# Performance work log

Hardware: AMD Instinct MI355X
Metric: run time of the kernel (lower is better)

Reference implementation:

```python
import jax, jax.numpy as jnp
from jax import lax
import numpy as np

LRELU_SLOPE = 0.01  # PyTorch LeakyReLU default
BETA = 0.25


def lrelu(x):
    return jnp.where(x >= 0, x, LRELU_SLOPE * x)


def conv2d(x, w, b, stride, pad):
    # x: [B,C,H,W], w: [Cout,Cin,k,k] (torch OIHW)
    y = lax.conv_general_dilated(x, w, (stride, stride), ((pad, pad), (pad, pad)),
                                 dimension_numbers=('NCHW', 'OIHW', 'NCHW'))
    return y + b[None, :, None, None]


def conv_transpose2d(x, w, b, stride, out_pad):
    # w: torch ConvTranspose2d weight [Cin,Cout,k,k]; implement as dilated conv
    # with spatially flipped kernel. out = (i-1)*stride + k + out_pad.
    wf = jnp.flip(w, (2, 3)).transpose(1, 0, 2, 3)  # -> [Cout,Cin,k,k]
    k = w.shape[2]
    pad = ((k - 1, k - 1 + out_pad), (k - 1, k - 1 + out_pad))
    y = lax.conv_general_dilated(x, wf, (1, 1), pad, lhs_dilation=(stride, stride),
                                 dimension_numbers=('NCHW', 'OIHW', 'NCHW'))
    return y + b[None, :, None, None]


def setup_inputs() -> dict:
    key = jax.random.key(0)
    ks = jax.random.split(key, 16)
    s = 0.05
    inp = {
        'x':   jax.random.normal(ks[0], (64, 1, 256, 256), jnp.float32),
        'ew1': jax.random.normal(ks[1], (8, 1, 4, 4), jnp.float32) * s,
        'eb1': jnp.zeros((8,), jnp.float32),
        'ew2': jax.random.normal(ks[2], (16, 8, 4, 4), jnp.float32) * s,
        'eb2': jnp.zeros((16,), jnp.float32),
        'ew3': jax.random.normal(ks[3], (32, 16, 4, 4), jnp.float32) * s,
        'eb3': jnp.zeros((32,), jnp.float32),
        'ew4': jax.random.normal(ks[4], (32, 32, 3, 3), jnp.float32) * s,
        'eb4': jnp.zeros((32,), jnp.float32),
        'ew5': jax.random.normal(ks[5], (64, 32, 1, 1), jnp.float32) * s,
        'eb5': jnp.zeros((64,), jnp.float32),
        'dw1': jax.random.normal(ks[6], (32, 64, 3, 3), jnp.float32) * s,
        'db1': jnp.zeros((32,), jnp.float32),
        'dw2': jax.random.normal(ks[7], (32, 16, 4, 4), jnp.float32) * s,
        'db2': jnp.zeros((16,), jnp.float32),
        'dw3': jax.random.normal(ks[8], (16, 8, 4, 4), jnp.float32) * s,
        'db3': jnp.zeros((8,), jnp.float32),
        'dw4': jax.random.normal(ks[9], (8, 1, 4, 4), jnp.float32) * s,
        'db4': jnp.zeros((1,), jnp.float32),
        # nn.init.uniform_(-1/K, 1/K) with K=512
        'codebook': jax.random.uniform(ks[10], (512, 64), jnp.float32,
                                       minval=-1.0 / 512, maxval=1.0 / 512),
    }
    return inp


def vqvae_forward(x, ew1, eb1, ew2, eb2, ew3, eb3, ew4, eb4, ew5, eb5,
                  dw1, db1, dw2, db2, dw3, db3, dw4, db4, codebook):
    # ---- encoder ----
    h = lrelu(conv2d(x, ew1, eb1, 2, 0))   # [B,8,127,127]
    h = lrelu(conv2d(h, ew2, eb2, 2, 0))   # [B,16,62,62]
    h = lrelu(conv2d(h, ew3, eb3, 2, 0))   # [B,32,30,30]
    h = lrelu(conv2d(h, ew4, eb4, 1, 1))   # [B,32,30,30]
    h = lrelu(conv2d(h, ew5, eb5, 1, 0))   # [B,64,30,30]
    # ---- vector quantizer ----
    lat = h.transpose(0, 2, 3, 1)                      # [B,h,w,D]
    D = lat.shape[-1]
    flat = lat.reshape(-1, D)                          # [N,D]
    # squared euclidean distances via expansion (same argmin as torch.norm)
    d2 = (jnp.sum(flat * flat, axis=1, keepdims=True)
          - 2.0 * flat @ codebook.T
          + jnp.sum(codebook * codebook, axis=1))      # [N,K]
    idx = jnp.argmin(d2, axis=1)                       # [N]
    q = codebook[idx].reshape(lat.shape)               # [B,h,w,D]
    commitment = jnp.mean((lax.stop_gradient(q) - lat) ** 2)
    embedding = jnp.mean((q - lax.stop_gradient(lat)) ** 2)
    vq_loss = commitment * BETA + embedding
    q_st = lat + lax.stop_gradient(q - lat)            # straight-through
    z = q_st.transpose(0, 3, 1, 2)                     # [B,D,h,w]
    # ---- decoder ----
    h = lrelu(conv2d(z, dw1, db1, 1, 1))               # [B,32,30,30]
    h = lrelu(conv_transpose2d(h, dw2, db2, 2, 1))     # [B,16,63,63]
    h = lrelu(conv_transpose2d(h, dw3, db3, 2, 1))     # [B,8,131,131]
    recons = jnp.tanh(conv_transpose2d(h, dw4, db4, 2, 0))  # [B,1,264,264]
    return recons, vq_loss


def reference(x, ew1, eb1, ew2, eb2, ew3, eb3, ew4, eb4, ew5, eb5,
              dw1, db1, dw2, db2, dw3, db3, dw4, db4, codebook):
    return vqvae_forward(x, ew1, eb1, ew2, eb2, ew3, eb3, ew4, eb4, ew5, eb5,
                         dw1, db1, dw2, db2, dw3, db3, dw4, db4, codebook)
```

## Files before the change

### kernel.cpp

```cpp
#include <hip/hip_runtime.h>
#include <hip/hip_bf16.h>
#include <math.h>

#define LRELU 0.01f

template<int NW>
__device__ __forceinline__ void ldw(const float* p, float* w) {
    if constexpr (NW % 4 == 0) {
#pragma unroll
        for (int u = 0; u < NW / 4; u++) {
            float4 v = *(const float4*)(p + 4 * u);
            w[4*u] = v.x; w[4*u+1] = v.y; w[4*u+2] = v.z; w[4*u+3] = v.w;
        }
    } else {
#pragma unroll
        for (int c = 0; c < NW; c++) w[c] = p[c];
    }
}

__device__ __forceinline__ void wfwd(const float* s, float* d, int CIN, int COUT,
                                     int KK, int i) {
    int co = i / (CIN * KK); int r = i - co * CIN * KK;
    int ci = r / KK; int t = r - ci * KK;
    d[(ci * KK + t) * COUT + co] = s[i];
}
__device__ __forceinline__ void wtr(const float* s, float* d, int CIN, int COUT,
                                    int KK, int i) {
    int ci = i / (COUT * KK); int r = i - ci * COUT * KK;
    int co = r / KK; int t = r - co * KK;
    d[(t * CIN + ci) * COUT + co] = s[i];
}
__global__ __launch_bounds__(256)
void prep_k(const float* e1, const float* e2, const float* e3, const float* e4,
            const float* e5, const float* d1, const float* d2, const float* d3,
            const float* d4, float* w, const float* cbp, float* hcbn,
            unsigned long long* keys, float* loss, int* idxm, int N) {
    int i = blockIdx.x * 256 + threadIdx.x;
    if      (i < 128)   wfwd(e1, w + 0,     1,  8, 16, i);
    else if (i < 2176)  wfwd(e2, w + 128,   8, 16, 16, i - 128);
    else if (i < 10368) wfwd(e3, w + 2176, 16, 32, 16, i - 2176);
    else if (i < 19584) wfwd(e4, w + 10368, 32, 32, 9, i - 10368);
    else if (i < 21632) wfwd(e5, w + 19584, 32, 64, 1, i - 19584);
    else if (i < 40064) wfwd(d1, w + 21632, 64, 32, 9, i - 21632);
    else if (i < 48256) wtr (d2, w + 40064, 32, 16, 16, i - 40064);
    else if (i < 50304) wtr (d3, w + 48256, 16,  8, 16, i - 48256);
    else if (i < 50432) wtr (d4, w + 50304,  8,  1, 16, i - 50304);
    else if (i < 50944) {
        int k = i - 50432;
        const float* c = cbp + k * 64;
        float s = 0.f;
#pragma unroll
        for (int d = 0; d < 64; d++) s = fmaf(c[d], c[d], s);
        hcbn[k] = 0.5f * s;
    } else if (i < 50944 + N) {
        keys[i - 50944] = 0xFFFFFFFFFFFFFFFFull;
    } else if (i == 50944 + N) {
        loss[0] = 0.f;
    } else if (i < 50945 + N + 64 * 124) {
        int j = i - (50945 + N);
        int b2 = j / 124, s = j - b2 * 124;
        int r, c;
        if (s < 32)      { r = 0;  c = s; }
        else if (s < 64) { r = 31; c = s - 32; }
        else { int u = s - 64; r = 1 + (u >> 1); c = (u & 1) * 31; }
        idxm[b2 * 1024 + r * 32 + c] = 512;
    }
}

__global__ __launch_bounds__(256)
void ubuild_k(const float* __restrict__ w, const float* __restrict__ cb,
              float* __restrict__ U) {
    int g = blockIdx.x * 256 + threadIdx.x;
    if (g >= 513 * 288) return;
    if (g >= 512 * 288) { U[g] = 0.f; return; }
    int k = g / 288, rem = g - k * 288;
    const float* cr = cb + k * 64;
    float s = 0.f;
#pragma unroll 4
    for (int ci = 0; ci < 64; ci++)
        s = fmaf(w[ci * 288 + rem], cr[ci], s);
    U[g] = s;
}

template<int CIN, int COUT, int CO_BLK, int HIN, int ISTR, int HOUT, int WOUT,
         int OPLANE, int OSTR, int OPAD, int CB, int RB, int ZCONV, int ZF_CH>
__global__ __launch_bounds__(256)
void convs2_k(const float* __restrict__ in, const float* __restrict__ wt,
              const float* __restrict__ bias, float* __restrict__ out) {
    const int b = blockIdx.x, cog = blockIdx.y, tid = threadIdx.x;
    if (ZF_CH > 0 && (int)blockIdx.z >= ZCONV) {
        if (cog != 0) return;
        int i = ((int)blockIdx.z - ZCONV) * 256 + tid;
        if (i >= ZF_CH * 124) return;
        int ch = i / 124, s = i - ch * 124;
        int r, c;
        if (s < 32)      { r = 0;  c = s; }
        else if (s < 64) { r = 31; c = s - 32; }
        else { int u = s - 64; r = 1 + (u >> 1); c = (u & 1) * 31; }
        out[(size_t)(b * ZF_CH + ch) * 1024 + r * 32 + c] = 0.f;
        return;
    }
    __shared__ __align__(16) float lw[CIN * 16 * CO_BLK];
    for (int i = tid; i < CIN * 16 * CO_BLK; i += 256) {
        int row = i / CO_BLK, c = i - row * CO_BLK;
        lw[i] = wt[row * COUT + cog * CO_BLK + c];
    }
    __syncthreads();

    const int tz = blockIdx.z;
    const int cbi = tz / RB, rb = tz - cbi * RB;
    const int tx = tid & 15, ty = tid >> 4;
    const int ow0 = (cbi * 16 + tx) * 2;
    const int oh  = rb * 16 + ty;
    if (oh >= HOUT || ow0 >= WOUT) return;
    const bool p1v = (ow0 + 1) < WOUT;

    float acc[CO_BLK][2];
#pragma unroll
    for (int c = 0; c < CO_BLK; c++) {
        float bv = bias[cog * CO_BLK + c];
        acc[c][0] = bv; acc[c][1] = bv;
    }
    const float* inb = in + ((size_t)(b * CIN) * HIN + oh * 2) * ISTR + ow0 * 2;
#pragma unroll 2
    for (int ci = 0; ci < CIN; ci++) {
        const float* r = inb + (size_t)ci * HIN * ISTR;
        float4 a4[4]; float2 b2[4];
#pragma unroll
        for (int kh = 0; kh < 4; kh++) {
            a4[kh] = *(const float4*)(r + kh * ISTR);
            b2[kh] = p1v ? *(const float2*)(r + kh * ISTR + 4) : make_float2(0.f, 0.f);
        }
        const float* wr = lw + ci * 16 * CO_BLK;
#pragma unroll
        for (int kh = 0; kh < 4; kh++) {
            float x0[4] = {a4[kh].x, a4[kh].y, a4[kh].z, a4[kh].w};
            float x1[4] = {a4[kh].z, a4[kh].w, b2[kh].x, b2[kh].y};
#pragma unroll
            for (int kw = 0; kw < 4; kw++) {
                float wv[CO_BLK];
                ldw<CO_BLK>(wr + (kh * 4 + kw) * CO_BLK, wv);
#pragma unroll
                for (int c = 0; c < CO_BLK; c++) {
                    acc[c][0] = fmaf(x0[kw], wv[c], acc[c][0]);
                    acc[c][1] = fmaf(x1[kw], wv[c], acc[c][1]);
                }
            }
        }
    }
    float* ob = out + (size_t)(b * COUT + cog * CO_BLK) * OPLANE
                    + (oh + OPAD) * OSTR + ow0 + OPAD;
#pragma unroll
    for (int c = 0; c < CO_BLK; c++) {
        float v0 = acc[c][0]; v0 = (v0 >= 0.f) ? v0 : LRELU * v0;
        ob[(size_t)c * OPLANE] = v0;
        if (p1v) {
            float v1 = acc[c][1]; v1 = (v1 >= 0.f) ? v1 : LRELU * v1;
            ob[(size_t)c * OPLANE + 1] = v1;
        }
    }
}

template<int CIN, int COUT, int CO_BLK, int OPLANE, int OSTR, int OPADH, int OPADV,
         bool ZSIDE>
__global__ __launch_bounds__(256)
void conv3_k(const float* __restrict__ in, const float* __restrict__ wt,
             const float* __restrict__ bias, float* __restrict__ out) {
    const int b = blockIdx.x, cog = blockIdx.y, tid = threadIdx.x;
    __shared__ __align__(16) float lw[CIN * 9 * CO_BLK];
    for (int i = tid; i < CIN * 9 * CO_BLK; i += 256) {
        int row = i / CO_BLK, c = i - row * CO_BLK;
        lw[i] = wt[row * COUT + cog * CO_BLK + c];
    }
    __syncthreads();

    const int rb = blockIdx.z;
    const int tx = tid & 15, ty = tid >> 4;
    const int r = rb * 16 + ty;
    if (r >= 30) return;
    const int ow0 = tx * 2;
    if (tx == 15) {
        if (ZSIDE) {
#pragma unroll
            for (int c = 0; c < CO_BLK; c++) {
                float* base = out + (size_t)(b * COUT + cog * CO_BLK + c) * OPLANE
                                  + (r + OPADV) * OSTR;
                base[0] = 0.f; base[31] = 0.f; base[32] = 0.f;
            }
        }
        return;
    }
    float acc[CO_BLK][2];
#pragma unroll
    for (int c = 0; c < CO_BLK; c++) {
        float bv = bias[cog * CO_BLK + c];
        acc[c][0] = bv; acc[c][1] = bv;
    }
    const float* inb = in + ((size_t)(b * CIN) * 32 + r) * 32 + ow0;
#pragma unroll 2
    for (int ci = 0; ci < CIN; ci++) {
        const float* rr = inb + (size_t)ci * 1024;
        float2 A[3], Bv[3];
#pragma unroll
        for (int kh = 0; kh < 3; kh++) {
            A[kh]  = *(const float2*)(rr + kh * 32);
            Bv[kh] = *(const float2*)(rr + kh * 32 + 2);
        }
        const float* wr = lw + ci * 9 * CO_BLK;
#pragma unroll
        for (int kh = 0; kh < 3; kh++) {
            float x0[3] = {A[kh].x, A[kh].y, Bv[kh].x};
            float x1[3] = {A[kh].y, Bv[kh].x, Bv[kh].y};
#pragma unroll
            for (int kw = 0; kw < 3; kw++) {
                float wv[CO_BLK];
                ldw<CO_BLK>(wr + (kh * 3 + kw) * CO_BLK, wv);
#pragma unroll
                for (int c = 0; c < CO_BLK; c++) {
                    acc[c][0] = fmaf(x0[kw], wv[c], acc[c][0]);
                    acc[c][1] = fmaf(x1[kw], wv[c], acc[c][1]);
                }
            }
        }
    }
    float* ob = out + (size_t)(b * COUT + cog * CO_BLK) * OPLANE
                    + (r + OPADV) * OSTR + ow0 + OPADH;
#pragma unroll
    for (int c = 0; c < CO_BLK; c++) {
        float v0 = acc[c][0]; v0 = (v0 >= 0.f) ? v0 : LRELU * v0;
        float v1 = acc[c][1]; v1 = (v1 >= 0.f) ? v1 : LRELU * v1;
        ob[(size_t)c * OPLANE] = v0;
        ob[(size_t)c * OPLANE + 1] = v1;
    }
}

template<int CIN, int COUT, int CO_BLK>
__global__ __launch_bounds__(256)
void conv1_k(const float* __restrict__ in, const float* __restrict__ wt,
             const float* __restrict__ bias, float* __restrict__ out) {
    __shared__ __align__(16) float lw[CIN * CO_BLK];
    const int b = blockIdx.x, cog = blockIdx.y;
    for (int i = threadIdx.x; i < CIN * CO_BLK; i += 256) {
        int row = i / CO_BLK, c = i - row * CO_BLK;
        lw[i] = wt[row * COUT + cog * CO_BLK + c];
    }
    __syncthreads();

    const int px4 = threadIdx.x * 4;
    float acc[CO_BLK][4];
#pragma unroll
    for (int c = 0; c < CO_BLK; c++) {
        float bv = bias[cog * CO_BLK + c];
        acc[c][0] = bv; acc[c][1] = bv; acc[c][2] = bv; acc[c][3] = bv;
    }
#pragma unroll 4
    for (int ci = 0; ci < CIN; ci++) {
        float4 x = *(const float4*)(in + (size_t)(b * CIN + ci) * 1024 + px4);
        float wv[CO_BLK];
        ldw<CO_BLK>(lw + ci * CO_BLK, wv);
#pragma unroll
        for (int c = 0; c < CO_BLK; c++) {
            acc[c][0] = fmaf(x.x, wv[c], acc[c][0]);
            acc[c][1] = fmaf(x.y, wv[c], acc[c][1]);
            acc[c][2] = fmaf(x.z, wv[c], acc[c][2]);
            acc[c][3] = fmaf(x.w, wv[c], acc[c][3]);
        }
    }
#pragma unroll
    for (int c = 0; c < CO_BLK; c++) {
        float4 v;
        v.x = (acc[c][0] >= 0.f) ? acc[c][0] : LRELU * acc[c][0];
        v.y = (acc[c][1] >= 0.f) ? acc[c][1] : LRELU * acc[c][1];
        v.z = (acc[c][2] >= 0.f) ? acc[c][2] : LRELU * acc[c][2];
        v.w = (acc[c][3] >= 0.f) ? acc[c][3] : LRELU * acc[c][3];
        *(float4*)(out + (size_t)(b * COUT + cog * CO_BLK + c) * 1024 + px4) = v;
    }
}

__global__ __launch_bounds__(256)
void d1tab_k(const int* __restrict__ idxm, const float* __restrict__ U,
             const float* __restrict__ bias, float* __restrict__ out) {
    const int b = blockIdx.x, cog = blockIdx.y, rt = blockIdx.z;
    const int tx = threadIdx.x & 31, ty = threadIdx.x >> 5;
    const int r = rt * 8 + ty;
    if (r >= 30) return;
    if (tx >= 30) {
        if (tx == 31) {
#pragma unroll
            for (int c = 0; c < 16; c++) {
                float* base = out + (size_t)(b * 32 + cog * 16 + c) * 1020 + r * 34;
                base[1] = 0.f; base[32] = 0.f; base[33] = 0.f;
            }
        }
        return;
    }
    const int* im = idxm + b * 1024 + r * 32 + tx;
    float acc[16];
#pragma unroll
    for (int c = 0; c < 16; c++) acc[c] = bias[cog * 16 + c];
#pragma unroll
    for (int kh = 0; kh < 3; kh++) {
        int i0 = im[kh * 32 + 0];
        int i1 = im[kh * 32 + 1];
        int i2 = im[kh * 32 + 2];
        const float4* u0 = (const float4*)(U + ((size_t)i0 * 9 + kh * 3 + 0) * 32 + cog * 16);
        const float4* u1 = (const float4*)(U + ((size_t)i1 * 9 + kh * 3 + 1) * 32 + cog * 16);
        const float4* u2 = (const float4*)(U + ((size_t)i2 * 9 + kh * 3 + 2) * 32 + cog * 16);
#pragma unroll
        for (int q = 0; q < 4; q++) {
            float4 a = u0[q], bb = u1[q], cc = u2[q];
            acc[4*q+0] += (a.x + bb.x) + cc.x;
            acc[4*q+1] += (a.y + bb.y) + cc.y;
            acc[4*q+2] += (a.z + bb.z) + cc.z;
            acc[4*q+3] += (a.w + bb.w) + cc.w;
        }
    }
    float* ob = out + (size_t)(b * 32 + cog * 16) * 1020 + r * 34 + tx + 2;
#pragma unroll
    for (int c = 0; c < 16; c++) {
        float v = acc[c]; v = (v >= 0.f) ? v : LRELU * v;
        ob[(size_t)c * 1020] = v;
    }
}

template<int CIN, int COUT, int CO_BLK, int HIN, int ISTR, int HOUT, int WOUT,
         int OPLANE, int OSTR, int OPADH, int NTX, int NT,
         int ZS_CH, int ZS_H, int ZS_STR, int ZC0, int ZC1, int ZC2,
         bool DO_TANH, bool DO_LOSS>
__global__ __launch_bounds__(256)
void convtf_k(const float* __restrict__ in, const float* __restrict__ wt,
              const float* __restrict__ bias, float* __restrict__ out,
              const float* __restrict__ loss, float* __restrict__ losstgt) {
    const int b = blockIdx.x, tid = threadIdx.x;
    const int NCOG = COUT / CO_BLK;
    int zz = blockIdx.z;
    if (zz >= NCOG * NT) {
        if (DO_LOSS) {
            if (b == 0 && tid == 0)
                losstgt[0] = 1.25f * loss[0] / (57600.f * 64.f);
            return;
        }
        int i = (zz - NCOG * NT) * 256 + tid;
        if (i >= ZS_CH * ZS_H * 3) return;
        int ch = i / (ZS_H * 3); int u = i - ch * ZS_H * 3;
        int r = u / 3, c3 = u - r * 3;
        int col = (c3 == 0) ? ZC0 : (c3 == 1) ? ZC1 : ZC2;
        out[((size_t)(b * ZS_CH + ch) * ZS_H + r) * ZS_STR + col] = 0.f;
        return;
    }
    const int cog = zz / NT, tile = zz - cog * NT;
    const int tlx = tile % NTX, tly = tile / NTX;

    __shared__ __align__(16) float lw[16 * CIN * CO_BLK];
    for (int i = tid; i < 16 * CIN * CO_BLK; i += 256) {
        int aq = i / (CIN * 4 * CO_BLK);
        int r1 = i - aq * (CIN * 4 * CO_BLK);
        int ci = r1 / (4 * CO_BLK);
        int u  = r1 - ci * (4 * CO_BLK);
        int pp = u / CO_BLK, c = u - pp * CO_BLK;
        int a = aq >> 1, q = aq & 1, py = pp >> 1, px = pp & 1;
        int tap = (py + 2 * a) * 4 + px + 2 * q;
        lw[i] = wt[((size_t)tap * CIN + ci) * COUT + cog * CO_BLK + c];
    }
    __syncthreads();

    const int SX = (WOUT + 1) >> 1, SY = (HOUT + 1) >> 1;
    const int sx0 = tlx * 32 + (tid & 15);
    const int sx1 = sx0 + 16;
    const int sy  = tly * 16 + (tid >> 4);
    const bool v0 = sx0 < SX, v1 = sx1 < SX;
    if (sy >= SY || !(v0 || v1)) return;

    const bool rvA = (sy < HIN);
    const bool rvB = (sy >= 1) && (sy <= HIN);

    float acc[2][4][CO_BLK];
#pragma unroll
    for (int s = 0; s < 2; s++)
#pragma unroll
        for (int o = 0; o < 4; o++)
#pragma unroll
            for (int c = 0; c < CO_BLK; c++)
                acc[s][o][c] = bias[cog * CO_BLK + c];

    const float* base = in + (size_t)(b * CIN) * HIN * ISTR;
#pragma unroll 2
    for (int ci = 0; ci < CIN; ci++) {
        const float* rowA = base + (size_t)ci * HIN * ISTR + (size_t)sy * ISTR;
        const float* rowB = rowA - ISTR;
        float rA0x = 0.f, rA0y = 0.f, rA1x = 0.f, rA1y = 0.f;
        float rB0x = 0.f, rB0y = 0.f, rB1x = 0.f, rB1y = 0.f;
        if (rvA) {
            if (v0) { rA0x = rowA[sx0]; rA0y = rowA[sx0 + 1]; }
            if (v1) { rA1x = rowA[sx1]; rA1y = rowA[sx1 + 1]; }
        }
        if (rvB) {
            if (v0) { rB0x = rowB[sx0]; rB0y = rowB[sx0 + 1]; }
            if (v1) { rB1x = rowB[sx1]; rB1y = rowB[sx1 + 1]; }
        }
#pragma unroll
        for (int a = 0; a < 2; a++) {
#pragma unroll
            for (int q = 0; q < 2; q++) {
                float iv0 = q ? (a ? rB0x : rA0x) : (a ? rB0y : rA0y);
                float iv1 = q ? (a ? rB1x : rA1x) : (a ? rB1y : rA1y);
                const float* wp = lw + (size_t)((a * 2 + q) * CIN + ci) * (4 * CO_BLK);
                float wv[4 * CO_BLK];
                ldw<4 * CO_BLK>(wp, wv);
#pragma unroll
                for (int o = 0; o < 4; o++)
#pragma unroll
                    for (int c = 0; c < CO_BLK; c++) {
                        acc[0][o][c] = fmaf(iv0, wv[o * CO_BLK + c], acc[0][o][c]);
                        acc[1][o][c] = fmaf(iv1, wv[o * CO_BLK + c], acc[1][o][c]);
                    }
            }
        }
    }
#pragma unroll
    for (int s = 0; s < 2; s++) {
        if (s ? !v1 : !v0) continue;
        const int sxx = s ? sx1 : sx0;
        const int ow = 2 * sxx;
        const bool full = (ow + 1) < WOUT;
#pragma unroll
        for (int py = 0; py < 2; py++) {
            int oh = 2 * sy + py;
            if (oh >= HOUT) continue;
            float* ob = out + (size_t)(b * COUT + cog * CO_BLK) * OPLANE
                            + (size_t)oh * OSTR + ow + OPADH;
#pragma unroll
            for (int c = 0; c < CO_BLK; c++) {
                float va = acc[s][py * 2 + 0][c];
                float vb = acc[s][py * 2 + 1][c];
                if (DO_TANH) { va = tanhf(va); vb = tanhf(vb); }
                else {
                    va = (va >= 0.f) ? va : LRELU * va;
                    vb = (vb >= 0.f) ? vb : LRELU * vb;
                }
                if ((OPADH & 1) == 0 && full) {
                    *(float2*)(ob + (size_t)c * OPLANE) = make_float2(va, vb);
                } else {
                    ob[(size_t)c * OPLANE] = va;
                    if (full) ob[(size_t)c * OPLANE + 1] = vb;
                }
            }
        }
    }
}

__global__ __launch_bounds__(256)
void vq_argmin_k(const float* __restrict__ lat, const float* __restrict__ cb,
                 const float* __restrict__ hcbn,
                 unsigned long long* __restrict__ keys) {
    const int pb = blockIdx.x;
    if (pb >= 225) return;
    __shared__ float4 scb4[1024];
    __shared__ float  shn[64];
    const int tid = threadIdx.x;
    const int dq  = tid & 3;
    const int pg  = tid >> 2;
    const int kbase = blockIdx.y * 64;
    const int posbase = pb * 256;

    const float4* src = (const float4*)(cb + (size_t)kbase * 64);
#pragma unroll
    for (int i = 0; i < 4; i++) scb4[tid + 256 * i] = src[tid + 256 * i];
    if (tid < 64) shn[tid] = hcbn[kbase + tid];

    float l[4][16];
    int   pidx[4];
#pragma unroll
    for (int j = 0; j < 4; j++) {
        int pos = posbase + pg + 64 * j;
        pidx[j] = pos;
        int b = pos / 900, p = pos - b * 900;
        int oh = p / 30, ow = p - oh * 30;
        int pp = 33 + oh * 32 + ow;
        const float* lb = lat + ((size_t)b * 64 + dq * 16) * 1024 + pp;
#pragma unroll
        for (int i = 0; i < 16; i++) l[j][i] = lb[i * 1024];
    }
    __syncthreads();

    float best[4] = {3.4e38f, 3.4e38f, 3.4e38f, 3.4e38f};
    int   bi[4]   = {0, 0, 0, 0};
#pragma unroll 2
    for (int k0 = 0; k0 < 64; k0++) {
        float4 c0 = scb4[k0 * 16 + dq * 4 + 0];
        float4 c1 = scb4[k0 * 16 + dq * 4 + 1];
        float4 c2 = scb4[k0 * 16 + dq * 4 + 2];
        float4 c3 = scb4[k0 * 16 + dq * 4 + 3];
        float hn = shn[k0];
#pragma unroll
        for (int j = 0; j < 4; j++) {
            float dot = 0.f;
            dot = fmaf(l[j][0],  c0.x, dot); dot = fmaf(l[j][1],  c0.y, dot);
            dot = fmaf(l[j][2],  c0.z, dot); dot = fmaf(l[j][3],  c0.w, dot);
            dot = fmaf(l[j][4],  c1.x, dot); dot = fmaf(l[j][5],  c1.y, dot);
            dot = fmaf(l[j][6],  c1.z, dot); dot = fmaf(l[j][7],  c1.w, dot);
            dot = fmaf(l[j][8],  c2.x, dot); dot = fmaf(l[j][9],  c2.y, dot);
            dot = fmaf(l[j][10], c2.z, dot); dot = fmaf(l[j][11], c2.w, dot);
            dot = fmaf(l[j][12], c3.x, dot); dot = fmaf(l[j][13], c3.y, dot);
            dot = fmaf(l[j][14], c3.z, dot); dot = fmaf(l[j][15], c3.w, dot);
            float full = dot + __shfl_xor(dot, 1);
            full += __shfl_xor(full, 2);
            float score = hn - full;
            if (score < best[j]) { best[j] = score; bi[j] = kbase + k0; }
        }
    }
    if (dq == 0) {
#pragma unroll
        for (int j = 0; j < 4; j++) {
            unsigned u = __float_as_uint(best[j]);
            u = ((int)u < 0) ? ~u : (u | 0x80000000u);
            unsigned long long key = ((unsigned long long)u << 32) | (unsigned)bi[j];
            atomicMin(&keys[pidx[j]], key);
        }
    }
}

__global__ __launch_bounds__(256)
void vq_finalize_k(const float* __restrict__ lat, const float* __restrict__ cb,
                   const unsigned long long* __restrict__ keys,
                   int* __restrict__ idxm, float* __restrict__ loss_acc, int B) {
    int gid = blockIdx.x * 256 + threadIdx.x;
    const int N = B * 900;
    float myloss = 0.f;
    if (gid < N) {
        int b = gid / 900, p = gid - b * 900;
        int oh = p / 30, ow = p - oh * 30;
        int pp = 33 + oh * 32 + ow;
        int idx = (int)(unsigned)(keys[gid] & 0xFFFFFFFFull);
        idxm[b * 1024 + pp] = idx;
        const float4* crow = (const float4*)(cb + (size_t)idx * 64);
        const float* lrow = lat + (size_t)b * 64 * 1024 + pp;
#pragma unroll
        for (int i = 0; i < 16; i++) {
            float4 cv = crow[i];
            float lv0 = lrow[(4 * i + 0) * 1024];
            float lv1 = lrow[(4 * i + 1) * 1024];
            float lv2 = lrow[(4 * i + 2) * 1024];
            float lv3 = lrow[(4 * i + 3) * 1024];
            float d0 = cv.x - lv0, d1 = cv.y - lv1, d2 = cv.z - lv2, d3 = cv.w - lv3;
            myloss = fmaf(d0, d0, myloss);
            myloss = fmaf(d1, d1, myloss);
            myloss = fmaf(d2, d2, myloss);
            myloss = fmaf(d3, d3, myloss);
        }
    }
    __shared__ float red[256];
    red[threadIdx.x] = myloss;
    __syncthreads();
    for (int s = 128; s > 0; s >>= 1) {
        if ((int)threadIdx.x < s) red[threadIdx.x] += red[threadIdx.x + s];
        __syncthreads();
    }
    if (threadIdx.x == 0) atomicAdd(loss_acc, red[0]);
}

static inline int nblk(long long total) { return (int)((total + 255) / 256); }

extern "C" void kernel_launch(void* const* d_in, const int* in_sizes, int n_in,
                              void* d_out, int out_size, void* d_ws, size_t ws_size,
                              hipStream_t stream) {
    const float* x   = (const float*)d_in[0];
    const float* ew1 = (const float*)d_in[1];  const float* eb1 = (const float*)d_in[2];
    const float* ew2 = (const float*)d_in[3];  const float* eb2 = (const float*)d_in[4];
    const float* ew3 = (const float*)d_in[5];  const float* eb3 = (const float*)d_in[6];
    const float* ew4 = (const float*)d_in[7];  const float* eb4 = (const float*)d_in[8];
    const float* ew5 = (const float*)d_in[9];  const float* eb5 = (const float*)d_in[10];
    const float* dw1 = (const float*)d_in[11]; const float* db1 = (const float*)d_in[12];
    const float* dw2 = (const float*)d_in[13]; const float* db2 = (const float*)d_in[14];
    const float* dw3 = (const float*)d_in[15]; const float* db3 = (const float*)d_in[16];
    const float* dw4 = (const float*)d_in[17]; const float* db4 = (const float*)d_in[18];
    const float* cb  = (const float*)d_in[19];
    float* out = (float*)d_out;

    const int B = in_sizes[0] / (256 * 256);
    const int N = B * 900;

    char* ws = (char*)d_ws;
    float* A     = (float*)(ws);
    float* Bb    = (float*)(ws + 34873344);
    float* d2out = (float*)(ws + 34873344);
    float* d3out = (float*)(ws);
    unsigned long long* keys = (unsigned long long*)(ws + 51126272);
    float* hcbn  = (float*)(ws + 51587072);
    int*   idxm  = (int*)(ws + 51589120);
    float* loss  = (float*)(ws + 52420608);
    float* wtb   = (float*)(ws + 52420864);
    float* U     = (float*)(ws + 52622592);
    float* ew1t = wtb;          float* ew2t = wtb + 128;
    float* ew3t = wtb + 2176;   float* ew4t = wtb + 10368;
    float* ew5t = wtb + 19584;  float* dw1t = wtb + 21632;
    float* dw2t = wtb + 40064;  float* dw3t = wtb + 48256;
    float* dw4t = wtb + 50304;

    prep_k<<<nblk(50945 + N + 64 * 124), 256, 0, stream>>>(
        ew1, ew2, ew3, ew4, ew5, dw1, dw2, dw3, dw4, wtb,
        cb, hcbn, keys, loss, idxm, N);
    ubuild_k<<<nblk(513 * 288), 256, 0, stream>>>(dw1t, cb, U);

    convs2_k<1, 8, 8, 256, 256, 127, 127, 127 * 128, 128, 0, 4, 8, 32, 0>
        <<<dim3(B, 1, 32), 256, 0, stream>>>(x, ew1t, eb1, A);
    convs2_k<8, 16, 4, 127, 128, 62, 62, 62 * 64, 64, 0, 2, 4, 8, 0>
        <<<dim3(B, 4, 8), 256, 0, stream>>>(A, ew2t, eb2, Bb);
    convs2_k<16, 32, 4, 62, 64, 30, 30, 1024, 32, 1, 1, 2, 2, 32>
        <<<dim3(B, 8, 18), 256, 0, stream>>>(Bb, ew3t, eb3, A);
    conv3_k<32, 32, 4, 1024, 32, 1, 1, false>
        <<<dim3(B, 8, 2), 256, 0, stream>>>(A, ew4t, eb4, Bb);
    conv1_k<32, 64, 4><<<dim3(B, 16, 1), 256, 0, stream>>>(Bb, ew5t, eb5, A);

    vq_argmin_k<<<dim3(232, 8), 256, 0, stream>>>(A, cb, hcbn, keys);
    vq_finalize_k<<<nblk(N), 256, 0, stream>>>(A, cb, keys, idxm, loss, B);

    d1tab_k<<<dim3(B, 2, 4), 256, 0, stream>>>(idxm, U, db1, A);
    convtf_k<32, 16, 4, 30, 34, 63, 63, 63 * 68, 68, 2, 1, 2,
             16, 63, 68, 1, 65, 66, false, false>
        <<<dim3(B, 1, 20), 256, 0, stream>>>(A + 1, dw2t, db2, d2out,
                                             nullptr, nullptr);
    convtf_k<16, 8, 8, 63, 68, 129, 129, 129 * 132, 132, 2, 3, 15,
             8, 129, 132, 1, 1, 131, false, false>
        <<<dim3(B, 1, 28), 256, 0, stream>>>(d2out + 1, dw3t, db3, d3out,
                                             nullptr, nullptr);
    convtf_k<8, 1, 1, 129, 132, 260, 260, 67600, 260, 0, 5, 45,
             0, 1, 1, 0, 0, 0, true, true>
        <<<dim3(B, 1, 46), 256, 0, stream>>>(d3out + 1, dw4t, db4, out, loss,
                                             out + (out_size - 1));
}
```

Before: 407.3 us.

## Fuse VQ finalize into argmin via last-block counter; specialize final deconv kernel

Removes the separate vq_finalize kernel: each position block increments a per-block counter after its atomicMin updates, and the last of the 8 codebook-slice blocks reads the final keys, writes idxm and accumulates the commitment loss using latents already held in registers. This saves a launch and a re-read of the latent tensor, at the cost of threadfence/atomic ordering and a counter array zeroed in prep. The last transposed conv (8->1 channels, tanh) moves to a dedicated d4_k kernel with a different tiling (28 tiles, 4 strips per thread), replacing the generic convtf instantiation.

```diff
diff --git a/kernel.cpp b/kernel.cpp
--- a/kernel.cpp
+++ b/kernel.cpp
@@ -34,7 +34,7 @@
 void prep_k(const float* e1, const float* e2, const float* e3, const float* e4,
             const float* e5, const float* d1, const float* d2, const float* d3,
             const float* d4, float* w, const float* cbp, float* hcbn,
-            unsigned long long* keys, float* loss, int* idxm, int N) {
+            unsigned long long* keys, float* loss, int* idxm, int* fincnt, int N) {
     int i = blockIdx.x * 256 + threadIdx.x;
     if      (i < 128)   wfwd(e1, w + 0,     1,  8, 16, i);
     else if (i < 2176)  wfwd(e2, w + 128,   8, 16, 16, i - 128);
@@ -64,6 +64,8 @@
         else if (s < 64) { r = 31; c = s - 32; }
         else { int u = s - 64; r = 1 + (u >> 1); c = (u & 1) * 31; }
         idxm[b2 * 1024 + r * 32 + c] = 512;
+    } else if (i < 50945 + N + 64 * 124 + 225) {
+        fincnt[i - (50945 + N + 64 * 124)] = 0;
     }
 }
 
@@ -326,20 +328,14 @@
 template<int CIN, int COUT, int CO_BLK, int HIN, int ISTR, int HOUT, int WOUT,
          int OPLANE, int OSTR, int OPADH, int NTX, int NT,
          int ZS_CH, int ZS_H, int ZS_STR, int ZC0, int ZC1, int ZC2,
-         bool DO_TANH, bool DO_LOSS>
+         bool DO_TANH>
 __global__ __launch_bounds__(256)
 void convtf_k(const float* __restrict__ in, const float* __restrict__ wt,
-              const float* __restrict__ bias, float* __restrict__ out,
-              const float* __restrict__ loss, float* __restrict__ losstgt) {
+              const float* __restrict__ bias, float* __restrict__ out) {
     const int b = blockIdx.x, tid = threadIdx.x;
     const int NCOG = COUT / CO_BLK;
     int zz = blockIdx.z;
     if (zz >= NCOG * NT) {
-        if (DO_LOSS) {
-            if (b == 0 && tid == 0)
-                losstgt[0] = 1.25f * loss[0] / (57600.f * 64.f);
-            return;
-        }
         int i = (zz - NCOG * NT) * 256 + tid;
         if (i >= ZS_CH * ZS_H * 3) return;
         int ch = i / (ZS_H * 3); int u = i - ch * ZS_H * 3;
@@ -450,13 +446,96 @@
 }
 
 __global__ __launch_bounds__(256)
+void d4_k(const float* __restrict__ in, const float* __restrict__ wt,
+          const float* __restrict__ bias, float* __restrict__ out,
+          const float* __restrict__ loss, float* __restrict__ losstgt) {
+    const int b = blockIdx.x, tid = threadIdx.x;
+    const int zz = blockIdx.z;
+    if (zz == 27) {
+        if (b == 0 && tid == 0)
+            losstgt[0] = 1.25f * loss[0] / (57600.f * 64.f);
+        return;
+    }
+    __shared__ __align__(16) float lw[128];
+    for (int i = tid; i < 128; i += 256) {
+        int aq = i >> 5, r = i & 31;
+        int ci = r >> 2, pp = r & 3;
+        int a = aq >> 1, q = aq & 1, py = pp >> 1, px = pp & 1;
+        int tap = (py + 2 * a) * 4 + px + 2 * q;
+        lw[i] = wt[tap * 8 + ci];
+    }
+    __syncthreads();
+    const int tlx = zz / 9, tly = zz - tlx * 9;
+    const int tx = tid & 15, ty = tid >> 4;
+    const int sy = tly * 16 + ty;
+    if (sy >= 130) return;
+    const int sxb = tlx * 64 + tx;
+    bool vs[4];
+    float acc[4][4];
+    const float bv = bias[0];
+#pragma unroll
+    for (int s = 0; s < 4; s++) {
+        vs[s] = (sxb + 16 * s) < 130;
+#pragma unroll
+        for (int o = 0; o < 4; o++) acc[s][o] = bv;
+    }
+    const bool rvA = (sy < 129);
+    const bool rvB = (sy >= 1);
+    const float* base = in + (size_t)(b * 8) * 129 * 132;
+#pragma unroll 2
+    for (int ci = 0; ci < 8; ci++) {
+        const float* rowA = base + (size_t)ci * 129 * 132 + (size_t)sy * 132;
+        const float* rowB = rowA - 132;
+        float ax[4], ay[4], bx[4], by[4];
+#pragma unroll
+        for (int s = 0; s < 4; s++) {
+            int sx = sxb + 16 * s;
+            bool v = vs[s];
+            ax[s] = (rvA && v) ? rowA[sx] : 0.f;
+            ay[s] = (rvA && v) ? rowA[sx + 1] : 0.f;
+            bx[s] = (rvB && v) ? rowB[sx] : 0.f;
+            by[s] = (rvB && v) ? rowB[sx + 1] : 0.f;
+        }
+#pragma unroll
+        for (int aq = 0; aq < 4; aq++) {
+            float wv[4];
+            ldw<4>(lw + aq * 32 + ci * 4, wv);
+            int a = aq >> 1, q = aq & 1;
+#pragma unroll
+            for (int s = 0; s < 4; s++) {
+                float iv = q ? (a ? bx[s] : ax[s]) : (a ? by[s] : ay[s]);
+#pragma unroll
+                for (int o = 0; o < 4; o++)
+                    acc[s][o] = fmaf(iv, wv[o], acc[s][o]);
+            }
+        }
+    }
+#pragma unroll
+    for (int s = 0; s < 4; s++) {
+        if (!vs[s]) continue;
+        int ow = 2 * (sxb + 16 * s);
+#pragma unroll
+        for (int py = 0; py < 2; py++) {
+            int oh = 2 * sy + py;
+            float va = tanhf(acc[s][py * 2 + 0]);
+            float vb = tanhf(acc[s][py * 2 + 1]);
+            *(float2*)(out + (size_t)b * 67600 + (size_t)oh * 260 + ow)
+                = make_float2(va, vb);
+        }
+    }
+}
+
+__global__ __launch_bounds__(256)
 void vq_argmin_k(const float* __restrict__ lat, const float* __restrict__ cb,
                  const float* __restrict__ hcbn,
-                 unsigned long long* __restrict__ keys) {
+                 unsigned long long* __restrict__ keys,
+                 int* __restrict__ idxm, float* __restrict__ loss_acc,
+                 int* __restrict__ fincnt) {
     const int pb = blockIdx.x;
     if (pb >= 225) return;
     __shared__ float4 scb4[1024];
     __shared__ float  shn[64];
+    __shared__ int lastFlag;
     const int tid = threadIdx.x;
     const int dq  = tid & 3;
     const int pg  = tid >> 2;
@@ -518,45 +597,51 @@
             atomicMin(&keys[pidx[j]], key);
         }
     }
-}
-
-__global__ __launch_bounds__(256)
-void vq_finalize_k(const float* __restrict__ lat, const float* __restrict__ cb,
-                   const unsigned long long* __restrict__ keys,
-                   int* __restrict__ idxm, float* __restrict__ loss_acc, int B) {
-    int gid = blockIdx.x * 256 + threadIdx.x;
-    const int N = B * 900;
+
+    __syncthreads();
+    if (tid == 0) {
+        __threadfence();
+        int prev = atomicAdd(&fincnt[pb], 1);
+        lastFlag = (prev == 7);
+    }
+    __syncthreads();
+    if (!lastFlag) return;
+    __threadfence();
+
+    float* red = (float*)scb4;
     float myloss = 0.f;
-    if (gid < N) {
-        int b = gid / 900, p = gid - b * 900;
-        int oh = p / 30, ow = p - oh * 30;
-        int pp = 33 + oh * 32 + ow;
-        int idx = (int)(unsigned)(keys[gid] & 0xFFFFFFFFull);
-        idxm[b * 1024 + pp] = idx;
-        const float4* crow = (const float4*)(cb + (size_t)idx * 64);
-        const float* lrow = lat + (size_t)b * 64 * 1024 + pp;
-#pragma unroll
-        for (int i = 0; i < 16; i++) {
+#pragma unroll
+    for (int j = 0; j < 4; j++) {
+        unsigned long long kv = __hip_atomic_load(&keys[pidx[j]], __ATOMIC_RELAXED,
+                                                  __HIP_MEMORY_SCOPE_AGENT);
+        int idx = (int)(unsigned)(kv & 0xFFFFFFFFull);
+        const float4* crow = (const float4*)(cb + (size_t)idx * 64 + dq * 16);
+#pragma unroll
+        for (int i = 0; i < 4; i++) {
             float4 cv = crow[i];
-            float lv0 = lrow[(4 * i + 0) * 1024];
-            float lv1 = lrow[(4 * i + 1) * 1024];
-            float lv2 = lrow[(4 * i + 2) * 1024];
-            float lv3 = lrow[(4 * i + 3) * 1024];
-            float d0 = cv.x - lv0, d1 = cv.y - lv1, d2 = cv.z - lv2, d3 = cv.w - lv3;
+            float d0 = cv.x - l[j][4*i+0];
+            float d1 = cv.y - l[j][4*i+1];
+            float d2 = cv.z - l[j][4*i+2];
+            float d3 = cv.w - l[j][4*i+3];
             myloss = fmaf(d0, d0, myloss);
             myloss = fmaf(d1, d1, myloss);
             myloss = fmaf(d2, d2, myloss);
             myloss = fmaf(d3, d3, myloss);
         }
-    }
-    __shared__ float red[256];
-    red[threadIdx.x] = myloss;
+        if (dq == 0) {
+            int pos = pidx[j];
+            int b = pos / 900, p = pos - b * 900;
+            int oh = p / 30, ow = p - oh * 30;
+            idxm[b * 1024 + 33 + oh * 32 + ow] = idx;
+        }
+    }
+    red[tid] = myloss;
     __syncthreads();
     for (int s = 128; s > 0; s >>= 1) {
-        if ((int)threadIdx.x < s) red[threadIdx.x] += red[threadIdx.x + s];
+        if (tid < s) red[tid] += red[tid + s];
         __syncthreads();
     }
-    if (threadIdx.x == 0) atomicAdd(loss_acc, red[0]);
+    if (tid == 0) atomicAdd(loss_acc, red[0]);
 }
 
 static inline int nblk(long long total) { return (int)((total + 255) / 256); }
@@ -588,6 +673,7 @@
     unsigned long long* keys = (unsigned long long*)(ws + 51126272);
     float* hcbn  = (float*)(ws + 51587072);
     int*   idxm  = (int*)(ws + 51589120);
+    int*   fincnt= (int*)(ws + 51851264);
     float* loss  = (float*)(ws + 52420608);
     float* wtb   = (float*)(ws + 52420864);
     float* U     = (float*)(ws + 52622592);
@@ -597,9 +683,9 @@
     float* dw2t = wtb + 40064;  float* dw3t = wtb + 48256;
     float* dw4t = wtb + 50304;
 
-    prep_k<<<nblk(50945 + N + 64 * 124), 256, 0, stream>>>(
+    prep_k<<<nblk(50945 + N + 64 * 124 + 225), 256, 0, stream>>>(
         ew1, ew2, ew3, ew4, ew5, dw1, dw2, dw3, dw4, wtb,
-        cb, hcbn, keys, loss, idxm, N);
+        cb, hcbn, keys, loss, idxm, fincnt, N);
     ubuild_k<<<nblk(513 * 288), 256, 0, stream>>>(dw1t, cb, U);
 
     convs2_k<1, 8, 8, 256, 256, 127, 127, 127 * 128, 128, 0, 4, 8, 32, 0>
@@ -612,20 +698,16 @@
         <<<dim3(B, 8, 2), 256, 0, stream>>>(A, ew4t, eb4, Bb);
     conv1_k<32, 64, 4><<<dim3(B, 16, 1), 256, 0, stream>>>(Bb, ew5t, eb5, A);
 
-    vq_argmin_k<<<dim3(232, 8), 256, 0, stream>>>(A, cb, hcbn, keys);
-    vq_finalize_k<<<nblk(N), 256, 0, stream>>>(A, cb, keys, idxm, loss, B);
+    vq_argmin_k<<<dim3(232, 8), 256, 0, stream>>>(A, cb, hcbn, keys,
+                                                  idxm, loss, fincnt);
 
     d1tab_k<<<dim3(B, 2, 4), 256, 0, stream>>>(idxm, U, db1, A);
     convtf_k<32, 16, 4, 30, 34, 63, 63, 63 * 68, 68, 2, 1, 2,
-             16, 63, 68, 1, 65, 66, false, false>
-        <<<dim3(B, 1, 20), 256, 0, stream>>>(A + 1, dw2t, db2, d2out,
-                                             nullptr, nullptr);
+             16, 63, 68, 1, 65, 66, false>
+        <<<dim3(B, 1, 20), 256, 0, stream>>>(A + 1, dw2t, db2, d2out);
     convtf_k<16, 8, 8, 63, 68, 129, 129, 129 * 132, 132, 2, 3, 15,
-             8, 129, 132, 1, 1, 131, false, false>
-        <<<dim3(B, 1, 28), 256, 0, stream>>>(d2out + 1, dw3t, db3, d3out,
-                                             nullptr, nullptr);
-    convtf_k<8, 1, 1, 129, 132, 260, 260, 67600, 260, 0, 5, 45,
-             0, 1, 1, 0, 0, 0, true, true>
-        <<<dim3(B, 1, 46), 256, 0, stream>>>(d3out + 1, dw4t, db4, out, loss,
+             8, 129, 132, 1, 1, 131, false>
+        <<<dim3(B, 1, 28), 256, 0, stream>>>(d2out + 1, dw3t, db3, d3out);
+    d4_k<<<dim3(B, 1, 28), 256, 0, stream>>>(d3out + 1, dw4t, db4, out, loss,
                                              out + (out_size - 1));
 }
```

New measurement: 429.3 us. 5.4% more time.
